# Kernel optimization log

Hardware: AMD Instinct MI355X
Metric: run time of the kernel (lower is better)

## Reference

```python
import jax, jax.numpy as jnp
import numpy as np
from jax import lax

SEQ_LEN, BATCH, POSE, H, PRED_LEN = 32, 32768, 34, 16, 15


def setup_inputs() -> dict:
    key = jax.random.key(0)
    ks = jax.random.split(key, 22)
    w = lambda k, s: (jax.random.normal(k, s, jnp.float32) * 0.1)
    return {
        "obs_s": jax.random.normal(ks[0], (SEQ_LEN, BATCH, POSE), jnp.float32),
        "enc_Wih": w(ks[1], (4 * H, POSE)), "enc_Whh": w(ks[2], (4 * H, H)),
        "enc_bih": w(ks[3], (4 * H,)), "enc_bhh": w(ks[4], (4 * H,)),
        "dec_Wih": w(ks[5], (4 * H, POSE)), "dec_Whh": w(ks[6], (4 * H, H)),
        "dec_bih": w(ks[7], (4 * H,)), "dec_bhh": w(ks[8], (4 * H,)),
        "cr_Wih": w(ks[9], (4 * H, POSE)), "cr_Whh": w(ks[10], (4 * H, H)),
        "cr_bih": w(ks[11], (4 * H,)), "cr_bhh": w(ks[12], (4 * H,)),
        "fc_W": w(ks[13], (POSE, H)), "fc_b": w(ks[14], (POSE,)),
        "fcc_W": w(ks[15], (2, H)), "fcc_b": w(ks[16], (2,)),
        "mlp_W": w(ks[17], (H, H)), "mlp_b": w(ks[18], (H,)),
        "emb_W": w(ks[19], (POSE, 2)), "emb_b": w(ks[20], (POSE,)),
        "pred_len": PRED_LEN,
    }


def _cell(x, h, c, Wih, Whh, bih, bhh):
    # torch LSTM gate order: i, f, g, o
    gates = x @ Wih.T + bih + h @ Whh.T + bhh  # [B, 4H]
    i, f, g, o = jnp.split(gates, 4, axis=-1)
    c = jax.nn.sigmoid(f) * c + jax.nn.sigmoid(i) * jnp.tanh(g)
    h = jax.nn.sigmoid(o) * jnp.tanh(c)
    return h, c


def reference(obs_s, enc_Wih, enc_Whh, enc_bih, enc_bhh,
              dec_Wih, dec_Whh, dec_bih, dec_bhh,
              cr_Wih, cr_Whh, cr_bih, cr_bhh,
              fc_W, fc_b, fcc_W, fcc_b, mlp_W, mlp_b, emb_W, emb_b,
              pred_len):
    batch = obs_s.shape[1]
    h0 = jnp.zeros((batch, H), obs_s.dtype)
    c0 = jnp.zeros((batch, H), obs_s.dtype)

    def enc_step(carry, x):
        h, c = _cell(x, *carry, enc_Wih, enc_Whh, enc_bih, enc_bhh)
        return (h, c), None

    (h, c), _ = lax.scan(enc_step, (h0, c0), obs_s)

    hc = h @ mlp_W.T + mlp_b           # crossing hidden init from encoder h
    cc = jnp.zeros_like(hc)
    last_s = obs_s[-1]                 # [B, POSE]
    last_cr = obs_s[-1]

    def dec_step(carry, _):
        h, c, hc, cc, last_s, last_cr = carry
        hc, cc = _cell(last_cr, hc, cc, cr_Wih, cr_Whh, cr_bih, cr_bhh)
        curr_cr = jax.nn.softmax(hc @ fcc_W.T + fcc_b, axis=-1)   # [B, 2]
        next_cr = curr_cr @ emb_W.T + emb_b                        # [B, POSE]
        h, c = _cell(last_s, h, c, dec_Wih, dec_Whh, dec_bih, dec_bhh)
        curr_s = h @ fc_W.T + fc_b                                 # [B, POSE]
        return (h, c, hc, cc, curr_s, next_cr), (curr_s, curr_cr)

    _, (pred_s, pred_crossing) = lax.scan(
        dec_step, (h, c, hc, cc, last_s, last_cr), None, length=pred_len)
    return pred_s, pred_crossing
```

## Files before the change

### kernel.cpp

```cpp
#include <hip/hip_runtime.h>
#include <cstddef>

#define SEQLEN 32
#define BATCH  32768
#define POSE   34
#define PREDL  15
#define LOG2E  1.4426950408889634f
#define K2E    2.8853901817779268f

typedef __attribute__((ext_vector_type(8))) short short8;
typedef __attribute__((ext_vector_type(4))) float f32x4;
typedef union { short8 s8; unsigned u[4]; } pk8;

#define MF(a,b,c) __builtin_amdgcn_mfma_f32_16x16x32_bf16(a,b,c,0,0,0)
#define EXP2(x)  __builtin_amdgcn_exp2f(x)
#define RCP(x)   __builtin_amdgcn_rcpf(x)

__device__ __forceinline__ unsigned short f2bf(float f){ __bf16 b=(__bf16)f; return __builtin_bit_cast(unsigned short,b); }
__device__ __forceinline__ unsigned f22bf(float lo,float hi){ return (unsigned)f2bf(lo) | ((unsigned)f2bf(hi)<<16); }
__device__ __forceinline__ short8 zero8(){ pk8 r; r.u[0]=0;r.u[1]=0;r.u[2]=0;r.u[3]=0; return r.s8; }
__device__ __forceinline__ float scGT(int gt){ return (gt==2)?K2E:LOG2E; }

__device__ __forceinline__ short8 g8s(const float* __restrict__ p, float s){
    pk8 r;
    r.u[0]=f22bf(p[0]*s,p[1]*s); r.u[1]=f22bf(p[2]*s,p[3]*s);
    r.u[2]=f22bf(p[4]*s,p[5]*s); r.u[3]=f22bf(p[6]*s,p[7]*s);
    return r.s8;
}

__device__ __forceinline__ void pw4v(const f32x4 (&ac)[4], f32x4 &cs,
                                     unsigned &hp0, unsigned &hp1){
    f32x4 A,C,B,O;
#pragma unroll
    for(int j=0;j<4;++j){
        A[j]=EXP2(-ac[0][j]); C[j]=EXP2(-ac[1][j]);
        B[j]=EXP2( ac[2][j]); O[j]=EXP2(-ac[3][j]);
    }
    const f32x4 one={1.f,1.f,1.f,1.f};
    f32x4 u=one+A, w=one+C, v=B+one, Bm=B-one;
    f32x4 t1=u*v;
    f32x4 num=cs*t1+Bm*w;
    f32x4 den=t1*w;
    f32x4 rd_,E,rh;
#pragma unroll
    for(int j=0;j<4;++j) rd_[j]=RCP(den[j]);
    f32x4 cn=num*rd_;
    cs=cn;
#pragma unroll
    for(int j=0;j<4;++j) E[j]=EXP2(K2E*cn[j]);
    f32x4 hd=(one+O)*(E+one);
#pragma unroll
    for(int j=0;j<4;++j) rh[j]=RCP(hd[j]);
    f32x4 hv=(E-one)*rh;
    hp0=f22bf(hv[0],hv[1]); hp1=f22bf(hv[2],hv[3]);
}

extern "C" __global__ void lstm_prep(
    const float* __restrict__ dWih, const float* __restrict__ dWhh,
    const float* __restrict__ dbih, const float* __restrict__ dbhh,
    const float* __restrict__ cWih, const float* __restrict__ cWhh,
    const float* __restrict__ cbih, const float* __restrict__ cbhh,
    const float* __restrict__ fcW,  const float* __restrict__ fcb,
    const float* __restrict__ embW, const float* __restrict__ embb,
    float* __restrict__ wsBD, float* __restrict__ wsBC,
    unsigned short* __restrict__ wsDh, unsigned short* __restrict__ wsCh,
    unsigned short* __restrict__ wsCp)
{
    int idx = blockIdx.x*256 + threadIdx.x;
    if(idx < 1024){
        int R=idx>>4, k=idx&15;
        float s=scGT(R>>4);
        float vD=dWhh[R*16+k];
        for(int p=0;p<34;++p) vD=fmaf(dWih[R*34+p],fcW[p*16+k],vD);
        wsDh[idx]=f2bf(vD*s);
        wsCh[idx]=f2bf(cWhh[R*16+k]*s);
    }
    if(idx < 128){
        int R=idx>>1, k=idx&1;
        float s=scGT(R>>4);
        float v=0.f;
        for(int p=0;p<34;++p) v=fmaf(cWih[R*34+p],embW[2*p+k],v);
        wsCp[idx]=f2bf(v*s);
    }
    if(idx < 64){
        int R=idx;
        float s=scGT(R>>4);
        float vD=dbih[R]+dbhh[R], vC=cbih[R]+cbhh[R];
        for(int p=0;p<34;++p){ vD=fmaf(dWih[R*34+p],fcb[p],vD); vC=fmaf(cWih[R*34+p],embb[p],vC); }
        wsBD[idx]=vD*s; wsBC[idx]=vC*s;
    }
}

extern "C" __global__ void __launch_bounds__(256,2) lstm_w7(
    const float* __restrict__ obs_s,
    const float* __restrict__ eWih, const float* __restrict__ eWhh,
    const float* __restrict__ ebih, const float* __restrict__ ebhh,
    const float* __restrict__ dWih, const float* __restrict__ dWhh,
    const float* __restrict__ dbih, const float* __restrict__ dbhh,
    const float* __restrict__ cWih, const float* __restrict__ cWhh,
    const float* __restrict__ cbih, const float* __restrict__ cbhh,
    const float* __restrict__ fcW,  const float* __restrict__ fcb,
    const float* __restrict__ fccW, const float* __restrict__ fccb,
    const float* __restrict__ mlpW, const float* __restrict__ mlpb,
    const float* __restrict__ wsBD, const float* __restrict__ wsBC,
    const unsigned short* __restrict__ wsDh, const unsigned short* __restrict__ wsCh,
    const unsigned short* __restrict__ wsCp,
    float* __restrict__ out_s, float* __restrict__ out_cr)
{
    __shared__ unsigned xt4[4][4][320];

    const int tid=threadIdx.x;
    const int l=tid&63;
    const int wv=tid>>6;
    const int lo=l&15, g=l>>4;
    const int pb=blockIdx.x*64 + wv*16;
    unsigned* XT=&xt4[wv][0][0];

    unsigned pofs[5]; int wofs[5];
#pragma unroll
    for(int it=0; it<5; ++it){
        int i2=l+64*it;
        int r=i2/17, w=i2-r*17;
        pofs[it]=(unsigned)((pb+r)*17+w);
        wofs[it]=r*20+w;
    }

    short8 wEx[4], wEhT[4]; f32x4 biasE[4];
#pragma unroll
    for(int gt=0;gt<4;++gt){
        float s=scGT(gt);
        int R=gt*16+lo;
        wEx[gt]=g8s(&eWih[R*34+8*g], s);
        pk8 r2;
        r2.u[0]=f22bf(eWhh[R*16+4*g]*s,   eWhh[R*16+4*g+1]*s);
        r2.u[1]=f22bf(eWhh[R*16+4*g+2]*s, eWhh[R*16+4*g+3]*s);
        r2.u[2]=(g==0)? f22bf(eWih[R*34+32]*s, eWih[R*34+33]*s) : 0u;
        r2.u[3]=0u;
        wEhT[gt]=r2.s8;
        float4 ba=*(const float4*)&ebih[gt*16+4*g];
        float4 bb=*(const float4*)&ebhh[gt*16+4*g];
        biasE[gt]=f32x4{(ba.x+bb.x)*s,(ba.y+bb.y)*s,(ba.z+bb.z)*s,(ba.w+bb.w)*s};
    }

    f32x4 cS={0.f,0.f,0.f,0.f};
    unsigned hp0=0u, hp1=0u;

    float2 RA[4][5];
    auto ldblk=[&](float2 (&R)[4][5], int t0){
#pragma unroll
        for(int s=0;s<4;++s){
            const float2* base=(const float2*)obs_s + (size_t)(t0+s)*(BATCH*17);
#pragma unroll
            for(int it=0;it<5;++it)
                if(it<4 || l<16) R[s][it]=base[pofs[it]];
        }
    };
    auto wrblk=[&](const float2 (&R)[4][5]){
#pragma unroll
        for(int s=0;s<4;++s)
#pragma unroll
            for(int it=0;it<5;++it)
                if(it<4 || l<16) XT[s*320+wofs[it]]=f22bf(R[s][it].x,R[s][it].y);
    };

    short8 fbQ=zero8(); unsigned ftQ=0u;
    ldblk(RA,0);
#pragma unroll 1
    for(int kb=0;kb<8;++kb){
        wrblk(RA);
        if(kb+1<8) ldblk(RA,4*(kb+1));
        short8 bx[4]; unsigned tw[4];
#pragma unroll
        for(int s=0;s<4;++s){
            bx[s]=*(const short8*)&XT[s*320+lo*20+4*g];
            tw[s]=XT[s*320+lo*20+16];
        }
        f32x4 cx[4][4];
#pragma unroll
        for(int s=0;s<4;++s)
#pragma unroll
            for(int gt=0;gt<4;++gt)
                cx[s][gt]=MF(wEx[gt],bx[s],biasE[gt]);
        fbQ=bx[3]; ftQ=tw[3];
#pragma unroll
        for(int s=0;s<4;++s){
            pk8 bh; bh.u[0]=hp0; bh.u[1]=hp1; bh.u[2]=(g==0)?tw[s]:0u; bh.u[3]=0u;
            f32x4 acc[4];
#pragma unroll
            for(int gt=0;gt<4;++gt) acc[gt]=MF(wEhT[gt],bh.s8,cx[s][gt]);
            pw4v(acc,cS,hp0,hp1);
        }
    }

    short8 wDh[4], wCA[4]; f32x4 biasD[4], biasC[4];
#pragma unroll
    for(int gt=0;gt<4;++gt){
        int R=gt*16+lo;
        uint2 qd=*(const uint2*)&wsDh[R*16+4*g];
        pk8 rd; rd.u[0]=qd.x; rd.u[1]=qd.y; rd.u[2]=0u; rd.u[3]=0u;
        wDh[gt]=rd.s8;
        uint2 qc=*(const uint2*)&wsCh[R*16+4*g];
        pk8 rc; rc.u[0]=qc.x; rc.u[1]=qc.y;
        rc.u[2]=(g==0)? *(const unsigned*)&wsCp[R*2] : 0u; rc.u[3]=0u;
        wCA[gt]=rc.s8;
        biasD[gt]=*(const f32x4*)&wsBD[gt*16+4*g];
        biasC[gt]=*(const f32x4*)&wsBC[gt*16+4*g];
    }
    short8 wF[3]; f32x4 fcbF[3];
#pragma unroll
    for(int nt=0;nt<3;++nt){
        int np=nt*16+lo;
        if(np<POSE){
            pk8 r;
            r.u[0]=f22bf(fcW[np*16+4*g],   fcW[np*16+4*g+1]);
            r.u[1]=f22bf(fcW[np*16+4*g+2], fcW[np*16+4*g+3]);
            r.u[2]=0u; r.u[3]=0u;
            wF[nt]=r.s8;
        } else wF[nt]=zero8();
#pragma unroll
        for(int j=0;j<4;++j){
            int row=nt*16+4*g+j;
            fcbF[nt][j]=(row<POSE)? fcb[row] : 0.f;
        }
    }
    short8 wFC, wM; f32x4 fccC, mlpbF;
    if(lo<2){
        pk8 r;
        r.u[0]=f22bf(fccW[lo*16+4*g],   fccW[lo*16+4*g+1]);
        r.u[1]=f22bf(fccW[lo*16+4*g+2], fccW[lo*16+4*g+3]);
        r.u[2]=0u; r.u[3]=0u; wFC=r.s8;
    } else wFC=zero8();
    fccC=(g==0)? f32x4{fccb[0],fccb[1],0.f,0.f} : f32x4{0.f,0.f,0.f,0.f};
    {
        pk8 r;
        r.u[0]=f22bf(mlpW[lo*16+4*g],   mlpW[lo*16+4*g+1]);
        r.u[1]=f22bf(mlpW[lo*16+4*g+2], mlpW[lo*16+4*g+3]);
        r.u[2]=0u; r.u[3]=0u; wM=r.s8;
        mlpbF=*(const f32x4*)&mlpb[4*g];
    }

    unsigned hcp0,hcp1;
    {
        pk8 bh; bh.u[0]=hp0; bh.u[1]=hp1; bh.u[2]=0u; bh.u[3]=0u;
        f32x4 o=MF(wM,bh.s8,mlpbF);
        hcp0=f22bf(o[0],o[1]); hcp1=f22bf(o[2],o[3]);
    }
    f32x4 cC={0.f,0.f,0.f,0.f};
    unsigned pp=0u;

    auto dec_tail=[&](int s, const f32x4 (&aC)[4], const f32x4 (&aD)[4]){
        pw4v(aD,cS,hp0,hp1);
        pw4v(aC,cC,hcp0,hcp1);
        pk8 bhc; bhc.u[0]=hcp0; bhc.u[1]=hcp1; bhc.u[2]=0u; bhc.u[3]=0u;
        f32x4 zz=MF(wFC,bhc.s8,fccC);
        float z0=zz[0], z1=zz[1];
        float mx=fmaxf(z0,z1);
        float e0=EXP2(LOG2E*(z0-mx)), e1=EXP2(LOG2E*(z1-mx));
        float rs=RCP(e0+e1);
        float p0=e0*rs, p1=e1*rs;
        unsigned ppn=f22bf(p0,p1);
        if(g==0)
            ((float2*)out_cr)[(size_t)s*BATCH+pb+lo]=make_float2(p0,p1);
        pp=(unsigned)__shfl((int)ppn, lo, 64);
        pk8 bh; bh.u[0]=hp0; bh.u[1]=hp1; bh.u[2]=0u; bh.u[3]=0u;
        float* po = out_s + ((size_t)s*BATCH + pb + lo)*POSE;
        f32x4 o0=MF(wF[0],bh.s8,fcbF[0]);
        f32x4 o1=MF(wF[1],bh.s8,fcbF[1]);
        *(float2*)(po+4*g)     =make_float2(o0[0],o0[1]);
        *(float2*)(po+4*g+2)   =make_float2(o0[2],o0[3]);
        *(float2*)(po+16+4*g)  =make_float2(o1[0],o1[1]);
        *(float2*)(po+16+4*g+2)=make_float2(o1[2],o1[3]);
        f32x4 o2=MF(wF[2],bh.s8,fcbF[2]);
        if(g==0) *(float2*)(po+32)=make_float2(o2[0],o2[1]);
    };

    {
        f32x4 aC[4], aD[4];
#pragma unroll
        for(int gt=0;gt<4;++gt){
            float s=scGT(gt);
            int R=gt*16+lo;
            short8 a1=g8s(&cWih[R*34+8*g], s);
            pk8 a2;
            a2.u[0]=f22bf(cWhh[R*16+4*g]*s,   cWhh[R*16+4*g+1]*s);
            a2.u[1]=f22bf(cWhh[R*16+4*g+2]*s, cWhh[R*16+4*g+3]*s);
            a2.u[2]=(g==0)? f22bf(cWih[R*34+32]*s, cWih[R*34+33]*s) : 0u;
            a2.u[3]=0u;
            float4 ba=*(const float4*)&cbih[gt*16+4*g];
            float4 bb=*(const float4*)&cbhh[gt*16+4*g];
            f32x4 bc0={(ba.x+bb.x)*s,(ba.y+bb.y)*s,(ba.z+bb.z)*s,(ba.w+bb.w)*s};
            pk8 bhc; bhc.u[0]=hcp0; bhc.u[1]=hcp1; bhc.u[2]=(g==0)?ftQ:0u; bhc.u[3]=0u;
            f32x4 cx=MF(a1,fbQ,bc0);
            aC[gt]=MF(a2.s8,bhc.s8,cx);
            short8 d1=g8s(&dWih[R*34+8*g], s);
            pk8 d2;
            d2.u[0]=f22bf(dWhh[R*16+4*g]*s,   dWhh[R*16+4*g+1]*s);
            d2.u[1]=f22bf(dWhh[R*16+4*g+2]*s, dWhh[R*16+4*g+3]*s);
            d2.u[2]=(g==0)? f22bf(dWih[R*34+32]*s, dWih[R*34+33]*s) : 0u;
            d2.u[3]=0u;
            float4 da=*(const float4*)&dbih[gt*16+4*g];
            float4 db=*(const float4*)&dbhh[gt*16+4*g];
            f32x4 bd0={(da.x+db.x)*s,(da.y+db.y)*s,(da.z+db.z)*s,(da.w+db.w)*s};
            pk8 bhd; bhd.u[0]=hp0; bhd.u[1]=hp1; bhd.u[2]=(g==0)?ftQ:0u; bhd.u[3]=0u;
            f32x4 dx=MF(d1,fbQ,bd0);
            aD[gt]=MF(d2.s8,bhd.s8,dx);
        }
        dec_tail(0,aC,aD);
    }
#pragma unroll 1
    for(int s=1;s<PREDL;++s){
        pk8 bd; bd.u[0]=hp0; bd.u[1]=hp1; bd.u[2]=0u; bd.u[3]=0u;
        pk8 bc; bc.u[0]=hcp0; bc.u[1]=hcp1; bc.u[2]=(g==0)?pp:0u; bc.u[3]=0u;
        f32x4 aC[4], aD[4];
#pragma unroll
        for(int gt=0;gt<4;++gt) aD[gt]=MF(wDh[gt],bd.s8,biasD[gt]);
#pragma unroll
        for(int gt=0;gt<4;++gt) aC[gt]=MF(wCA[gt],bc.s8,biasC[gt]);
        dec_tail(s,aC,aD);
    }
}

extern "C" void kernel_launch(void* const* d_in, const int* in_sizes, int n_in,
                              void* d_out, int out_size, void* d_ws, size_t ws_size,
                              hipStream_t stream)
{
    const float* obs  = (const float*)d_in[0];
    const float* eWih = (const float*)d_in[1];
    const float* eWhh = (const float*)d_in[2];
    const float* ebih = (const float*)d_in[3];
    const float* ebhh = (const float*)d_in[4];
    const float* dWih = (const float*)d_in[5];
    const float* dWhh = (const float*)d_in[6];
    const float* dbih = (const float*)d_in[7];
    const float* dbhh = (const float*)d_in[8];
    const float* cWih = (const float*)d_in[9];
    const float* cWhh = (const float*)d_in[10];
    const float* cbih = (const float*)d_in[11];
    const float* cbhh = (const float*)d_in[12];
    const float* fcW  = (const float*)d_in[13];
    const float* fcb  = (const float*)d_in[14];
    const float* fccW = (const float*)d_in[15];
    const float* fccb = (const float*)d_in[16];
    const float* mlpW = (const float*)d_in[17];
    const float* mlpb = (const float*)d_in[18];
    const float* embW = (const float*)d_in[19];
    const float* embb = (const float*)d_in[20];

    float* out_s  = (float*)d_out;
    float* out_cr = out_s + (size_t)PREDL*BATCH*POSE;

    float* wsBD = (float*)d_ws;
    float* wsBC = wsBD + 64;
    unsigned short* wsDh = (unsigned short*)(wsBC+64);
    unsigned short* wsCh = wsDh + 1024;
    unsigned short* wsCp = wsCh + 1024;

    hipLaunchKernelGGL(lstm_prep, dim3(4), dim3(256), 0, stream,
                       dWih, dWhh, dbih, dbhh, cWih, cWhh, cbih, cbhh,
                       fcW, fcb, embW, embb, wsBD, wsBC, wsDh, wsCh, wsCp);
    hipLaunchKernelGGL(lstm_w7, dim3(BATCH/64), dim3(256), 0, stream,
                       obs, eWih, eWhh, ebih, ebhh, dWih, dWhh, dbih, dbhh,
                       cWih, cWhh, cbih, cbhh, fcW, fcb, fccW, fccb,
                       mlpW, mlpb, wsBD, wsBC, wsDh, wsCh, wsCp,
                       out_s, out_cr);
}
```

Baseline: 66.67 us.

## Process two independent 16-row batch chunks per wave to interleave LSTM recurrences

Each wave now handles two 16-sample chunks instead of one, so the grid shrinks to half the blocks and the recurrent MFMA and pointwise gate chains of the two chunks are interleaved. This is meant to hide the serial latency of the per-step MFMA to exp/rcp to MFMA dependency chain through instruction-level parallelism within a wave. The cost is more registers (launch bounds drop to one block per SIMD pair), fewer resident waves, and a different observation load and LDS staging layout (two timesteps per block instead of four).

```diff
diff --git a/kernel.cpp b/kernel.cpp
--- a/kernel.cpp
+++ b/kernel.cpp
@@ -28,31 +28,36 @@
     return r.s8;
 }
 
-__device__ __forceinline__ void pw4v(const f32x4 (&ac)[4], f32x4 &cs,
-                                     unsigned &hp0, unsigned &hp1){
-    f32x4 A,C,B,O;
+__device__ __forceinline__ void pw4v2(const f32x4 (&ac)[2][4], f32x4 (&cs)[2],
+                                      unsigned (&hp0)[2], unsigned (&hp1)[2]){
+    f32x4 A[2],C[2],B[2],O[2];
+#pragma unroll
+    for(int ch=0;ch<2;++ch)
 #pragma unroll
     for(int j=0;j<4;++j){
-        A[j]=EXP2(-ac[0][j]); C[j]=EXP2(-ac[1][j]);
-        B[j]=EXP2( ac[2][j]); O[j]=EXP2(-ac[3][j]);
+        A[ch][j]=EXP2(-ac[ch][0][j]); C[ch][j]=EXP2(-ac[ch][1][j]);
+        B[ch][j]=EXP2( ac[ch][2][j]); O[ch][j]=EXP2(-ac[ch][3][j]);
     }
     const f32x4 one={1.f,1.f,1.f,1.f};
-    f32x4 u=one+A, w=one+C, v=B+one, Bm=B-one;
-    f32x4 t1=u*v;
-    f32x4 num=cs*t1+Bm*w;
-    f32x4 den=t1*w;
-    f32x4 rd_,E,rh;
-#pragma unroll
-    for(int j=0;j<4;++j) rd_[j]=RCP(den[j]);
-    f32x4 cn=num*rd_;
-    cs=cn;
-#pragma unroll
-    for(int j=0;j<4;++j) E[j]=EXP2(K2E*cn[j]);
-    f32x4 hd=(one+O)*(E+one);
-#pragma unroll
-    for(int j=0;j<4;++j) rh[j]=RCP(hd[j]);
-    f32x4 hv=(E-one)*rh;
-    hp0=f22bf(hv[0],hv[1]); hp1=f22bf(hv[2],hv[3]);
+#pragma unroll
+    for(int ch=0;ch<2;++ch){
+        f32x4 u=one+A[ch], w=one+C[ch], v=B[ch]+one, Bm=B[ch]-one;
+        f32x4 t1=u*v;
+        f32x4 num=cs[ch]*t1+Bm*w;
+        f32x4 den=t1*w;
+        f32x4 rd_,E,rh;
+#pragma unroll
+        for(int j=0;j<4;++j) rd_[j]=RCP(den[j]);
+        f32x4 cn=num*rd_;
+        cs[ch]=cn;
+#pragma unroll
+        for(int j=0;j<4;++j) E[j]=EXP2(K2E*cn[j]);
+        f32x4 hd=(one+O[ch])*(E+one);
+#pragma unroll
+        for(int j=0;j<4;++j) rh[j]=RCP(hd[j]);
+        f32x4 hv=(E-one)*rh;
+        hp0[ch]=f22bf(hv[0],hv[1]); hp1[ch]=f22bf(hv[2],hv[3]);
+    }
 }
 
 extern "C" __global__ void lstm_prep(
@@ -91,7 +96,7 @@
     }
 }
 
-extern "C" __global__ void __launch_bounds__(256,2) lstm_w7(
+extern "C" __global__ void __launch_bounds__(256,1) lstm_w8(
     const float* __restrict__ obs_s,
     const float* __restrict__ eWih, const float* __restrict__ eWhh,
     const float* __restrict__ ebih, const float* __restrict__ ebhh,
@@ -107,14 +112,14 @@
     const unsigned short* __restrict__ wsCp,
     float* __restrict__ out_s, float* __restrict__ out_cr)
 {
-    __shared__ unsigned xt4[4][4][320];
+    __shared__ unsigned xt4[4][2][2][320];
 
     const int tid=threadIdx.x;
     const int l=tid&63;
     const int wv=tid>>6;
     const int lo=l&15, g=l>>4;
-    const int pb=blockIdx.x*64 + wv*16;
-    unsigned* XT=&xt4[wv][0][0];
+    const int pb=blockIdx.x*128 + wv*32;
+    unsigned (*XT)[2][320]=xt4[wv];
 
     unsigned pofs[5]; int wofs[5];
 #pragma unroll
@@ -142,53 +147,67 @@
         biasE[gt]=f32x4{(ba.x+bb.x)*s,(ba.y+bb.y)*s,(ba.z+bb.z)*s,(ba.w+bb.w)*s};
     }
 
-    f32x4 cS={0.f,0.f,0.f,0.f};
-    unsigned hp0=0u, hp1=0u;
-
-    float2 RA[4][5];
-    auto ldblk=[&](float2 (&R)[4][5], int t0){
-#pragma unroll
-        for(int s=0;s<4;++s){
-            const float2* base=(const float2*)obs_s + (size_t)(t0+s)*(BATCH*17);
+    f32x4 cS[2]={{0.f,0.f,0.f,0.f},{0.f,0.f,0.f,0.f}};
+    unsigned hp0[2]={0u,0u}, hp1[2]={0u,0u};
+
+    float2 RA[2][2][5];
+    auto ldblk=[&](int t0){
+#pragma unroll
+        for(int s2=0;s2<2;++s2){
+            const float2* base=(const float2*)obs_s + (size_t)(t0+s2)*(BATCH*17);
+#pragma unroll
+            for(int ch=0;ch<2;++ch)
 #pragma unroll
             for(int it=0;it<5;++it)
-                if(it<4 || l<16) R[s][it]=base[pofs[it]];
+                if(it<4 || l<16) RA[ch][s2][it]=base[pofs[it]+ch*272u];
         }
     };
-    auto wrblk=[&](const float2 (&R)[4][5]){
-#pragma unroll
-        for(int s=0;s<4;++s)
-#pragma unroll
-            for(int it=0;it<5;++it)
-                if(it<4 || l<16) XT[s*320+wofs[it]]=f22bf(R[s][it].x,R[s][it].y);
+    auto wrblk=[&](){
+#pragma unroll
+        for(int ch=0;ch<2;++ch)
+#pragma unroll
+        for(int s2=0;s2<2;++s2)
+#pragma unroll
+        for(int it=0;it<5;++it)
+            if(it<4 || l<16) XT[ch][s2][wofs[it]]=f22bf(RA[ch][s2][it].x,RA[ch][s2][it].y);
     };
 
-    short8 fbQ=zero8(); unsigned ftQ=0u;
-    ldblk(RA,0);
+    short8 fbQ[2]; unsigned ftQ[2];
+    fbQ[0]=zero8(); fbQ[1]=zero8(); ftQ[0]=0u; ftQ[1]=0u;
+    ldblk(0);
 #pragma unroll 1
-    for(int kb=0;kb<8;++kb){
-        wrblk(RA);
-        if(kb+1<8) ldblk(RA,4*(kb+1));
-        short8 bx[4]; unsigned tw[4];
-#pragma unroll
-        for(int s=0;s<4;++s){
-            bx[s]=*(const short8*)&XT[s*320+lo*20+4*g];
-            tw[s]=XT[s*320+lo*20+16];
-        }
-        f32x4 cx[4][4];
-#pragma unroll
-        for(int s=0;s<4;++s)
-#pragma unroll
-            for(int gt=0;gt<4;++gt)
-                cx[s][gt]=MF(wEx[gt],bx[s],biasE[gt]);
-        fbQ=bx[3]; ftQ=tw[3];
-#pragma unroll
-        for(int s=0;s<4;++s){
-            pk8 bh; bh.u[0]=hp0; bh.u[1]=hp1; bh.u[2]=(g==0)?tw[s]:0u; bh.u[3]=0u;
-            f32x4 acc[4];
-#pragma unroll
-            for(int gt=0;gt<4;++gt) acc[gt]=MF(wEhT[gt],bh.s8,cx[s][gt]);
-            pw4v(acc,cS,hp0,hp1);
+    for(int kb=0;kb<16;++kb){
+        wrblk();
+        if(kb+1<16) ldblk(2*(kb+1));
+        short8 bx[2][2]; unsigned tw[2][2];
+#pragma unroll
+        for(int ch=0;ch<2;++ch)
+#pragma unroll
+        for(int s2=0;s2<2;++s2){
+            bx[ch][s2]=*(const short8*)&XT[ch][s2][lo*20+4*g];
+            tw[ch][s2]=XT[ch][s2][lo*20+16];
+        }
+        f32x4 cx[2][2][4];
+#pragma unroll
+        for(int ch=0;ch<2;++ch)
+#pragma unroll
+        for(int s2=0;s2<2;++s2)
+#pragma unroll
+        for(int gt=0;gt<4;++gt)
+            cx[ch][s2][gt]=MF(wEx[gt],bx[ch][s2],biasE[gt]);
+        fbQ[0]=bx[0][1]; ftQ[0]=tw[0][1];
+        fbQ[1]=bx[1][1]; ftQ[1]=tw[1][1];
+#pragma unroll
+        for(int s2=0;s2<2;++s2){
+            f32x4 acc[2][4];
+#pragma unroll
+            for(int ch=0;ch<2;++ch){
+                pk8 bh; bh.u[0]=hp0[ch]; bh.u[1]=hp1[ch];
+                bh.u[2]=(g==0)?tw[ch][s2]:0u; bh.u[3]=0u;
+#pragma unroll
+                for(int gt=0;gt<4;++gt) acc[ch][gt]=MF(wEhT[gt],bh.s8,cx[ch][s2][gt]);
+            }
+            pw4v2(acc,cS,hp0,hp1);
         }
     }
 
@@ -239,83 +258,104 @@
         mlpbF=*(const f32x4*)&mlpb[4*g];
     }
 
-    unsigned hcp0,hcp1;
+    unsigned hcp0[2],hcp1[2];
+#pragma unroll
+    for(int ch=0;ch<2;++ch){
+        pk8 bh; bh.u[0]=hp0[ch]; bh.u[1]=hp1[ch]; bh.u[2]=0u; bh.u[3]=0u;
+        f32x4 o=MF(wM,bh.s8,mlpbF);
+        hcp0[ch]=f22bf(o[0],o[1]); hcp1[ch]=f22bf(o[2],o[3]);
+    }
+    f32x4 cC[2]={{0.f,0.f,0.f,0.f},{0.f,0.f,0.f,0.f}};
+    unsigned pp[2]={0u,0u};
+
+    auto dec_tail=[&](int s, const f32x4 (&aC)[2][4], const f32x4 (&aD)[2][4]){
+        pw4v2(aD,cS,hp0,hp1);
+        pw4v2(aC,cC,hcp0,hcp1);
+#pragma unroll
+        for(int ch=0;ch<2;++ch){
+            const int pbc=pb+16*ch;
+            pk8 bhc; bhc.u[0]=hcp0[ch]; bhc.u[1]=hcp1[ch]; bhc.u[2]=0u; bhc.u[3]=0u;
+            f32x4 zz=MF(wFC,bhc.s8,fccC);
+            float z0=zz[0], z1=zz[1];
+            float mx=fmaxf(z0,z1);
+            float e0=EXP2(LOG2E*(z0-mx)), e1=EXP2(LOG2E*(z1-mx));
+            float rs=RCP(e0+e1);
+            float p0=e0*rs, p1=e1*rs;
+            unsigned ppn=f22bf(p0,p1);
+            if(g==0)
+                ((float2*)out_cr)[(size_t)s*BATCH+pbc+lo]=make_float2(p0,p1);
+            pp[ch]=(unsigned)__shfl((int)ppn, lo, 64);
+            pk8 bh; bh.u[0]=hp0[ch]; bh.u[1]=hp1[ch]; bh.u[2]=0u; bh.u[3]=0u;
+            float* po = out_s + ((size_t)s*BATCH + pbc + lo)*POSE;
+            f32x4 o0=MF(wF[0],bh.s8,fcbF[0]);
+            f32x4 o1=MF(wF[1],bh.s8,fcbF[1]);
+            *(float2*)(po+4*g)     =make_float2(o0[0],o0[1]);
+            *(float2*)(po+4*g+2)   =make_float2(o0[2],o0[3]);
+            *(float2*)(po+16+4*g)  =make_float2(o1[0],o1[1]);
+            *(float2*)(po+16+4*g+2)=make_float2(o1[2],o1[3]);
+            f32x4 o2=MF(wF[2],bh.s8,fcbF[2]);
+            if(g==0) *(float2*)(po+32)=make_float2(o2[0],o2[1]);
+        }
+    };
+
     {
-        pk8 bh; bh.u[0]=hp0; bh.u[1]=hp1; bh.u[2]=0u; bh.u[3]=0u;
-        f32x4 o=MF(wM,bh.s8,mlpbF);
-        hcp0=f22bf(o[0],o[1]); hcp1=f22bf(o[2],o[3]);
-    }
-    f32x4 cC={0.f,0.f,0.f,0.f};
-    unsigned pp=0u;
-
-    auto dec_tail=[&](int s, const f32x4 (&aC)[4], const f32x4 (&aD)[4]){
-        pw4v(aD,cS,hp0,hp1);
-        pw4v(aC,cC,hcp0,hcp1);
-        pk8 bhc; bhc.u[0]=hcp0; bhc.u[1]=hcp1; bhc.u[2]=0u; bhc.u[3]=0u;
-        f32x4 zz=MF(wFC,bhc.s8,fccC);
-        float z0=zz[0], z1=zz[1];
-        float mx=fmaxf(z0,z1);
-        float e0=EXP2(LOG2E*(z0-mx)), e1=EXP2(LOG2E*(z1-mx));
-        float rs=RCP(e0+e1);
-        float p0=e0*rs, p1=e1*rs;
-        unsigned ppn=f22bf(p0,p1);
-        if(g==0)
-            ((float2*)out_cr)[(size_t)s*BATCH+pb+lo]=make_float2(p0,p1);
-        pp=(unsigned)__shfl((int)ppn, lo, 64);
-        pk8 bh; bh.u[0]=hp0; bh.u[1]=hp1; bh.u[2]=0u; bh.u[3]=0u;
-        float* po = out_s + ((size_t)s*BATCH + pb + lo)*POSE;
-        f32x4 o0=MF(wF[0],bh.s8,fcbF[0]);
-        f32x4 o1=MF(wF[1],bh.s8,fcbF[1]);
-        *(float2*)(po+4*g)     =make_float2(o0[0],o0[1]);
-        *(float2*)(po+4*g+2)   =make_float2(o0[2],o0[3]);
-        *(float2*)(po+16+4*g)  =make_float2(o1[0],o1[1]);
-        *(float2*)(po+16+4*g+2)=make_float2(o1[2],o1[3]);
-        f32x4 o2=MF(wF[2],bh.s8,fcbF[2]);
-        if(g==0) *(float2*)(po+32)=make_float2(o2[0],o2[1]);
-    };
-
-    {
-        f32x4 aC[4], aD[4];
+        short8 a1c[4],a2c[4],a1d[4],a2d[4]; f32x4 bc0[4],bd0[4];
 #pragma unroll
         for(int gt=0;gt<4;++gt){
-            float s=scGT(gt);
+            float sgt=scGT(gt);
             int R=gt*16+lo;
-            short8 a1=g8s(&cWih[R*34+8*g], s);
+            a1c[gt]=g8s(&cWih[R*34+8*g], sgt);
             pk8 a2;
-            a2.u[0]=f22bf(cWhh[R*16+4*g]*s,   cWhh[R*16+4*g+1]*s);
-            a2.u[1]=f22bf(cWhh[R*16+4*g+2]*s, cWhh[R*16+4*g+3]*s);
-            a2.u[2]=(g==0)? f22bf(cWih[R*34+32]*s, cWih[R*34+33]*s) : 0u;
+            a2.u[0]=f22bf(cWhh[R*16+4*g]*sgt,   cWhh[R*16+4*g+1]*sgt);
+            a2.u[1]=f22bf(cWhh[R*16+4*g+2]*sgt, cWhh[R*16+4*g+3]*sgt);
+            a2.u[2]=(g==0)? f22bf(cWih[R*34+32]*sgt, cWih[R*34+33]*sgt) : 0u;
             a2.u[3]=0u;
+            a2c[gt]=a2.s8;
             float4 ba=*(const float4*)&cbih[gt*16+4*g];
             float4 bb=*(const float4*)&cbhh[gt*16+4*g];
-            f32x4 bc0={(ba.x+bb.x)*s,(ba.y+bb.y)*s,(ba.z+bb.z)*s,(ba.w+bb.w)*s};
-            pk8 bhc; bhc.u[0]=hcp0; bhc.u[1]=hcp1; bhc.u[2]=(g==0)?ftQ:0u; bhc.u[3]=0u;
-            f32x4 cx=MF(a1,fbQ,bc0);
-            aC[gt]=MF(a2.s8,bhc.s8,cx);
-            short8 d1=g8s(&dWih[R*34+8*g], s);
+            bc0[gt]=f32x4{(ba.x+bb.x)*sgt,(ba.y+bb.y)*sgt,(ba.z+bb.z)*sgt,(ba.w+bb.w)*sgt};
+            a1d[gt]=g8s(&dWih[R*34+8*g], sgt);
             pk8 d2;
-            d2.u[0]=f22bf(dWhh[R*16+4*g]*s,   dWhh[R*16+4*g+1]*s);
-            d2.u[1]=f22bf(dWhh[R*16+4*g+2]*s, dWhh[R*16+4*g+3]*s);
-            d2.u[2]=(g==0)? f22bf(dWih[R*34+32]*s, dWih[R*34+33]*s) : 0u;
+            d2.u[0]=f22bf(dWhh[R*16+4*g]*sgt,   dWhh[R*16+4*g+1]*sgt);
+            d2.u[1]=f22bf(dWhh[R*16+4*g+2]*sgt, dWhh[R*16+4*g+3]*sgt);
+            d2.u[2]=(g==0)? f22bf(dWih[R*34+32]*sgt, dWih[R*34+33]*sgt) : 0u;
             d2.u[3]=0u;
+            a2d[gt]=d2.s8;
             float4 da=*(const float4*)&dbih[gt*16+4*g];
             float4 db=*(const float4*)&dbhh[gt*16+4*g];
-            f32x4 bd0={(da.x+db.x)*s,(da.y+db.y)*s,(da.z+db.z)*s,(da.w+db.w)*s};
-            pk8 bhd; bhd.u[0]=hp0; bhd.u[1]=hp1; bhd.u[2]=(g==0)?ftQ:0u; bhd.u[3]=0u;
-            f32x4 dx=MF(d1,fbQ,bd0);
-            aD[gt]=MF(d2.s8,bhd.s8,dx);
+            bd0[gt]=f32x4{(da.x+db.x)*sgt,(da.y+db.y)*sgt,(da.z+db.z)*sgt,(da.w+db.w)*sgt};
+        }
+        f32x4 aC[2][4], aD[2][4];
+#pragma unroll
+        for(int ch=0;ch<2;++ch){
+            pk8 bhc; bhc.u[0]=hcp0[ch]; bhc.u[1]=hcp1[ch];
+            bhc.u[2]=(g==0)?ftQ[ch]:0u; bhc.u[3]=0u;
+            pk8 bhd; bhd.u[0]=hp0[ch]; bhd.u[1]=hp1[ch];
+            bhd.u[2]=(g==0)?ftQ[ch]:0u; bhd.u[3]=0u;
+#pragma unroll
+            for(int gt=0;gt<4;++gt){
+                f32x4 cxx=MF(a1c[gt],fbQ[ch],bc0[gt]);
+                aC[ch][gt]=MF(a2c[gt],bhc.s8,cxx);
+                f32x4 dxx=MF(a1d[gt],fbQ[ch],bd0[gt]);
+                aD[ch][gt]=MF(a2d[gt],bhd.s8,dxx);
+            }
         }
         dec_tail(0,aC,aD);
     }
 #pragma unroll 1
     for(int s=1;s<PREDL;++s){
-        pk8 bd; bd.u[0]=hp0; bd.u[1]=hp1; bd.u[2]=0u; bd.u[3]=0u;
-        pk8 bc; bc.u[0]=hcp0; bc.u[1]=hcp1; bc.u[2]=(g==0)?pp:0u; bc.u[3]=0u;
-        f32x4 aC[4], aD[4];
-#pragma unroll
-        for(int gt=0;gt<4;++gt) aD[gt]=MF(wDh[gt],bd.s8,biasD[gt]);
-#pragma unroll
-        for(int gt=0;gt<4;++gt) aC[gt]=MF(wCA[gt],bc.s8,biasC[gt]);
+        f32x4 aC[2][4], aD[2][4];
+#pragma unroll
+        for(int ch=0;ch<2;++ch){
+            pk8 bd; bd.u[0]=hp0[ch]; bd.u[1]=hp1[ch]; bd.u[2]=0u; bd.u[3]=0u;
+            pk8 bc; bc.u[0]=hcp0[ch]; bc.u[1]=hcp1[ch];
+            bc.u[2]=(g==0)?pp[ch]:0u; bc.u[3]=0u;
+#pragma unroll
+            for(int gt=0;gt<4;++gt){
+                aD[ch][gt]=MF(wDh[gt],bd.s8,biasD[gt]);
+                aC[ch][gt]=MF(wCA[gt],bc.s8,biasC[gt]);
+            }
+        }
         dec_tail(s,aC,aD);
     }
 }
@@ -358,7 +398,7 @@
     hipLaunchKernelGGL(lstm_prep, dim3(4), dim3(256), 0, stream,
                        dWih, dWhh, dbih, dbhh, cWih, cWhh, cbih, cbhh,
                        fcW, fcb, embW, embb, wsBD, wsBC, wsDh, wsCh, wsCp);
-    hipLaunchKernelGGL(lstm_w7, dim3(BATCH/64), dim3(256), 0, stream,
+    hipLaunchKernelGGL(lstm_w8, dim3(BATCH/128), dim3(256), 0, stream,
                        obs, eWih, eWhh, ebih, ebhh, dWih, dWhh, dbih, dbhh,
                        cWih, cWhh, cbih, cbhh, fcW, fcb, fccW, fccb,
                        mlpW, mlpb, wsBD, wsBC, wsDh, wsCh, wsCp,
```

Result: slower. 74.79 us (+12.2%).

## Split encoder and decoder kernels; run decoder and crossing LSTMs on separate waves

Applied to the files above, without the earlier changes.

The fused kernel is split in two. An encoder kernel also runs the weight-prep work in one extra block and writes each lane's h, hc and c state to workspace. A decoder kernel then gives the decoder LSTM and the crossing LSTM to different wavefronts, so their two independent recurrences run in parallel across twice as many waves. This doubles the decoder grid and shortens the serial chain per wave. The cost is a global round-trip for the state, an extra launch boundary, and a re-read of the last observation frame.

```diff
diff --git a/kernel.cpp b/kernel.cpp
--- a/kernel.cpp
+++ b/kernel.cpp
@@ -55,7 +55,11 @@
     hp0=f22bf(hv[0],hv[1]); hp1=f22bf(hv[2],hv[3]);
 }
 
-extern "C" __global__ void lstm_prep(
+extern "C" __global__ void __launch_bounds__(256,2) lstm_enc(
+    const float* __restrict__ obs_s,
+    const float* __restrict__ eWih, const float* __restrict__ eWhh,
+    const float* __restrict__ ebih, const float* __restrict__ ebhh,
+    const float* __restrict__ mlpW, const float* __restrict__ mlpb,
     const float* __restrict__ dWih, const float* __restrict__ dWhh,
     const float* __restrict__ dbih, const float* __restrict__ dbhh,
     const float* __restrict__ cWih, const float* __restrict__ cWhh,
@@ -64,50 +68,35 @@
     const float* __restrict__ embW, const float* __restrict__ embb,
     float* __restrict__ wsBD, float* __restrict__ wsBC,
     unsigned short* __restrict__ wsDh, unsigned short* __restrict__ wsCh,
-    unsigned short* __restrict__ wsCp)
-{
-    int idx = blockIdx.x*256 + threadIdx.x;
-    if(idx < 1024){
-        int R=idx>>4, k=idx&15;
-        float s=scGT(R>>4);
-        float vD=dWhh[R*16+k];
-        for(int p=0;p<34;++p) vD=fmaf(dWih[R*34+p],fcW[p*16+k],vD);
-        wsDh[idx]=f2bf(vD*s);
-        wsCh[idx]=f2bf(cWhh[R*16+k]*s);
-    }
-    if(idx < 128){
-        int R=idx>>1, k=idx&1;
-        float s=scGT(R>>4);
-        float v=0.f;
-        for(int p=0;p<34;++p) v=fmaf(cWih[R*34+p],embW[2*p+k],v);
-        wsCp[idx]=f2bf(v*s);
-    }
-    if(idx < 64){
-        int R=idx;
-        float s=scGT(R>>4);
-        float vD=dbih[R]+dbhh[R], vC=cbih[R]+cbhh[R];
-        for(int p=0;p<34;++p){ vD=fmaf(dWih[R*34+p],fcb[p],vD); vC=fmaf(cWih[R*34+p],embb[p],vC); }
-        wsBD[idx]=vD*s; wsBC[idx]=vC*s;
-    }
-}
-
-extern "C" __global__ void __launch_bounds__(256,2) lstm_w7(
-    const float* __restrict__ obs_s,
-    const float* __restrict__ eWih, const float* __restrict__ eWhh,
-    const float* __restrict__ ebih, const float* __restrict__ ebhh,
-    const float* __restrict__ dWih, const float* __restrict__ dWhh,
-    const float* __restrict__ dbih, const float* __restrict__ dbhh,
-    const float* __restrict__ cWih, const float* __restrict__ cWhh,
-    const float* __restrict__ cbih, const float* __restrict__ cbhh,
-    const float* __restrict__ fcW,  const float* __restrict__ fcb,
-    const float* __restrict__ fccW, const float* __restrict__ fccb,
-    const float* __restrict__ mlpW, const float* __restrict__ mlpb,
-    const float* __restrict__ wsBD, const float* __restrict__ wsBC,
-    const unsigned short* __restrict__ wsDh, const unsigned short* __restrict__ wsCh,
-    const unsigned short* __restrict__ wsCp,
-    float* __restrict__ out_s, float* __restrict__ out_cr)
+    unsigned short* __restrict__ wsCp, unsigned* __restrict__ hand)
 {
     __shared__ unsigned xt4[4][4][320];
+
+    if(blockIdx.x>=512){
+        for(int idx=threadIdx.x; idx<1024; idx+=256){
+            int R=idx>>4, k=idx&15;
+            float s=scGT(R>>4);
+            float vD=dWhh[R*16+k];
+            for(int p=0;p<34;++p) vD=fmaf(dWih[R*34+p],fcW[p*16+k],vD);
+            wsDh[idx]=f2bf(vD*s);
+            wsCh[idx]=f2bf(cWhh[R*16+k]*s);
+        }
+        for(int idx=threadIdx.x; idx<128; idx+=256){
+            int R=idx>>1, k=idx&1;
+            float s=scGT(R>>4);
+            float v=0.f;
+            for(int p=0;p<34;++p) v=fmaf(cWih[R*34+p],embW[2*p+k],v);
+            wsCp[idx]=f2bf(v*s);
+        }
+        for(int idx=threadIdx.x; idx<64; idx+=256){
+            int R=idx;
+            float s=scGT(R>>4);
+            float vD=dbih[R]+dbhh[R], vC=cbih[R]+cbhh[R];
+            for(int p=0;p<34;++p){ vD=fmaf(dWih[R*34+p],fcb[p],vD); vC=fmaf(cWih[R*34+p],embb[p],vC); }
+            wsBD[idx]=vD*s; wsBC[idx]=vC*s;
+        }
+        return;
+    }
 
     const int tid=threadIdx.x;
     const int l=tid&63;
@@ -146,29 +135,28 @@
     unsigned hp0=0u, hp1=0u;
 
     float2 RA[4][5];
-    auto ldblk=[&](float2 (&R)[4][5], int t0){
+    auto ldblk=[&](int t0){
 #pragma unroll
         for(int s=0;s<4;++s){
             const float2* base=(const float2*)obs_s + (size_t)(t0+s)*(BATCH*17);
 #pragma unroll
             for(int it=0;it<5;++it)
-                if(it<4 || l<16) R[s][it]=base[pofs[it]];
+                if(it<4 || l<16) RA[s][it]=base[pofs[it]];
         }
     };
-    auto wrblk=[&](const float2 (&R)[4][5]){
+    auto wrblk=[&](){
 #pragma unroll
         for(int s=0;s<4;++s)
 #pragma unroll
             for(int it=0;it<5;++it)
-                if(it<4 || l<16) XT[s*320+wofs[it]]=f22bf(R[s][it].x,R[s][it].y);
+                if(it<4 || l<16) XT[s*320+wofs[it]]=f22bf(RA[s][it].x,RA[s][it].y);
     };
 
-    short8 fbQ=zero8(); unsigned ftQ=0u;
-    ldblk(RA,0);
+    ldblk(0);
 #pragma unroll 1
     for(int kb=0;kb<8;++kb){
-        wrblk(RA);
-        if(kb+1<8) ldblk(RA,4*(kb+1));
+        wrblk();
+        if(kb+1<8) ldblk(4*(kb+1));
         short8 bx[4]; unsigned tw[4];
 #pragma unroll
         for(int s=0;s<4;++s){
@@ -181,7 +169,6 @@
 #pragma unroll
             for(int gt=0;gt<4;++gt)
                 cx[s][gt]=MF(wEx[gt],bx[s],biasE[gt]);
-        fbQ=bx[3]; ftQ=tw[3];
 #pragma unroll
         for(int s=0;s<4;++s){
             pk8 bh; bh.u[0]=hp0; bh.u[1]=hp1; bh.u[2]=(g==0)?tw[s]:0u; bh.u[3]=0u;
@@ -192,131 +179,188 @@
         }
     }
 
-    short8 wDh[4], wCA[4]; f32x4 biasD[4], biasC[4];
-#pragma unroll
-    for(int gt=0;gt<4;++gt){
-        int R=gt*16+lo;
-        uint2 qd=*(const uint2*)&wsDh[R*16+4*g];
-        pk8 rd; rd.u[0]=qd.x; rd.u[1]=qd.y; rd.u[2]=0u; rd.u[3]=0u;
-        wDh[gt]=rd.s8;
-        uint2 qc=*(const uint2*)&wsCh[R*16+4*g];
-        pk8 rc; rc.u[0]=qc.x; rc.u[1]=qc.y;
-        rc.u[2]=(g==0)? *(const unsigned*)&wsCp[R*2] : 0u; rc.u[3]=0u;
-        wCA[gt]=rc.s8;
-        biasD[gt]=*(const f32x4*)&wsBD[gt*16+4*g];
-        biasC[gt]=*(const f32x4*)&wsBC[gt*16+4*g];
-    }
-    short8 wF[3]; f32x4 fcbF[3];
-#pragma unroll
-    for(int nt=0;nt<3;++nt){
-        int np=nt*16+lo;
-        if(np<POSE){
-            pk8 r;
-            r.u[0]=f22bf(fcW[np*16+4*g],   fcW[np*16+4*g+1]);
-            r.u[1]=f22bf(fcW[np*16+4*g+2], fcW[np*16+4*g+3]);
-            r.u[2]=0u; r.u[3]=0u;
-            wF[nt]=r.s8;
-        } else wF[nt]=zero8();
-#pragma unroll
-        for(int j=0;j<4;++j){
-            int row=nt*16+4*g+j;
-            fcbF[nt][j]=(row<POSE)? fcb[row] : 0.f;
-        }
-    }
-    short8 wFC, wM; f32x4 fccC, mlpbF;
-    if(lo<2){
-        pk8 r;
-        r.u[0]=f22bf(fccW[lo*16+4*g],   fccW[lo*16+4*g+1]);
-        r.u[1]=f22bf(fccW[lo*16+4*g+2], fccW[lo*16+4*g+3]);
-        r.u[2]=0u; r.u[3]=0u; wFC=r.s8;
-    } else wFC=zero8();
-    fccC=(g==0)? f32x4{fccb[0],fccb[1],0.f,0.f} : f32x4{0.f,0.f,0.f,0.f};
+    unsigned hcp0,hcp1;
     {
         pk8 r;
         r.u[0]=f22bf(mlpW[lo*16+4*g],   mlpW[lo*16+4*g+1]);
         r.u[1]=f22bf(mlpW[lo*16+4*g+2], mlpW[lo*16+4*g+3]);
-        r.u[2]=0u; r.u[3]=0u; wM=r.s8;
-        mlpbF=*(const f32x4*)&mlpb[4*g];
-    }
-
-    unsigned hcp0,hcp1;
+        r.u[2]=0u; r.u[3]=0u;
+        f32x4 mb=*(const f32x4*)&mlpb[4*g];
+        pk8 bh; bh.u[0]=hp0; bh.u[1]=hp1; bh.u[2]=0u; bh.u[3]=0u;
+        f32x4 o=MF(r.s8,bh.s8,mb);
+        hcp0=f22bf(o[0],o[1]); hcp1=f22bf(o[2],o[3]);
+    }
+
+    unsigned* Hw = hand + ((size_t)(blockIdx.x*4+wv)*64 + l)*8;
+    Hw[0]=hp0; Hw[1]=hp1; Hw[2]=hcp0; Hw[3]=hcp1;
+    *(f32x4*)(Hw+4)=cS;
+}
+
+extern "C" __global__ void __launch_bounds__(256,2) lstm_dec(
+    const float* __restrict__ obs_s,
+    const float* __restrict__ dWih, const float* __restrict__ dWhh,
+    const float* __restrict__ dbih, const float* __restrict__ dbhh,
+    const float* __restrict__ cWih, const float* __restrict__ cWhh,
+    const float* __restrict__ cbih, const float* __restrict__ cbhh,
+    const float* __restrict__ fcW,  const float* __restrict__ fcb,
+    const float* __restrict__ fccW, const float* __restrict__ fccb,
+    const float* __restrict__ wsBD, const float* __restrict__ wsBC,
+    const unsigned short* __restrict__ wsDh, const unsigned short* __restrict__ wsCh,
+    const unsigned short* __restrict__ wsCp, const unsigned* __restrict__ hand,
+    float* __restrict__ out_s, float* __restrict__ out_cr)
+{
+    const int tid=threadIdx.x;
+    const int l=tid&63;
+    const int wv=tid>>6;
+    const int lo=l&15, g=l>>4;
+    const int grp=blockIdx.x*2+(wv>>1);
+    const int role=__builtin_amdgcn_readfirstlane(wv&1);
+    const int pb=grp*16;
+
+    const unsigned* H = hand + ((size_t)grp*64 + l)*8;
+    unsigned h0w=H[0], h1w=H[1], hc0w=H[2], hc1w=H[3];
+    f32x4 csIn=*(const f32x4*)(H+4);
+
+    const float* px=obs_s+((size_t)(SEQLEN-1)*BATCH+pb+lo)*POSE;
+    short8 fbQ;
     {
-        pk8 bh; bh.u[0]=hp0; bh.u[1]=hp1; bh.u[2]=0u; bh.u[3]=0u;
-        f32x4 o=MF(wM,bh.s8,mlpbF);
-        hcp0=f22bf(o[0],o[1]); hcp1=f22bf(o[2],o[3]);
-    }
-    f32x4 cC={0.f,0.f,0.f,0.f};
-    unsigned pp=0u;
-
-    auto dec_tail=[&](int s, const f32x4 (&aC)[4], const f32x4 (&aD)[4]){
-        pw4v(aD,cS,hp0,hp1);
-        pw4v(aC,cC,hcp0,hcp1);
-        pk8 bhc; bhc.u[0]=hcp0; bhc.u[1]=hcp1; bhc.u[2]=0u; bhc.u[3]=0u;
-        f32x4 zz=MF(wFC,bhc.s8,fccC);
-        float z0=zz[0], z1=zz[1];
-        float mx=fmaxf(z0,z1);
-        float e0=EXP2(LOG2E*(z0-mx)), e1=EXP2(LOG2E*(z1-mx));
-        float rs=RCP(e0+e1);
-        float p0=e0*rs, p1=e1*rs;
-        unsigned ppn=f22bf(p0,p1);
-        if(g==0)
-            ((float2*)out_cr)[(size_t)s*BATCH+pb+lo]=make_float2(p0,p1);
-        pp=(unsigned)__shfl((int)ppn, lo, 64);
-        pk8 bh; bh.u[0]=hp0; bh.u[1]=hp1; bh.u[2]=0u; bh.u[3]=0u;
-        float* po = out_s + ((size_t)s*BATCH + pb + lo)*POSE;
-        f32x4 o0=MF(wF[0],bh.s8,fcbF[0]);
-        f32x4 o1=MF(wF[1],bh.s8,fcbF[1]);
-        *(float2*)(po+4*g)     =make_float2(o0[0],o0[1]);
-        *(float2*)(po+4*g+2)   =make_float2(o0[2],o0[3]);
-        *(float2*)(po+16+4*g)  =make_float2(o1[0],o1[1]);
-        *(float2*)(po+16+4*g+2)=make_float2(o1[2],o1[3]);
-        f32x4 o2=MF(wF[2],bh.s8,fcbF[2]);
-        if(g==0) *(float2*)(po+32)=make_float2(o2[0],o2[1]);
-    };
-
-    {
-        f32x4 aC[4], aD[4];
+        const float2* p2=(const float2*)(px+8*g);
+        float2 q0=p2[0],q1=p2[1],q2=p2[2],q3=p2[3];
+        pk8 r;
+        r.u[0]=f22bf(q0.x,q0.y); r.u[1]=f22bf(q1.x,q1.y);
+        r.u[2]=f22bf(q2.x,q2.y); r.u[3]=f22bf(q3.x,q3.y);
+        fbQ=r.s8;
+    }
+    unsigned ftQ=f22bf(px[32],px[33]);
+
+    if(role==0){
+        f32x4 cS=csIn;
+        unsigned hp0=h0w, hp1=h1w;
+        f32x4 aD[4];
+        {
+#pragma unroll
+            for(int gt=0;gt<4;++gt){
+                float s=scGT(gt);
+                int R=gt*16+lo;
+                short8 d1=g8s(&dWih[R*34+8*g], s);
+                pk8 d2;
+                d2.u[0]=f22bf(dWhh[R*16+4*g]*s,   dWhh[R*16+4*g+1]*s);
+                d2.u[1]=f22bf(dWhh[R*16+4*g+2]*s, dWhh[R*16+4*g+3]*s);
+                d2.u[2]=(g==0)? f22bf(dWih[R*34+32]*s, dWih[R*34+33]*s) : 0u;
+                d2.u[3]=0u;
+                float4 da=*(const float4*)&dbih[gt*16+4*g];
+                float4 db=*(const float4*)&dbhh[gt*16+4*g];
+                f32x4 bd0={(da.x+db.x)*s,(da.y+db.y)*s,(da.z+db.z)*s,(da.w+db.w)*s};
+                pk8 bhd; bhd.u[0]=hp0; bhd.u[1]=hp1; bhd.u[2]=(g==0)?ftQ:0u; bhd.u[3]=0u;
+                f32x4 dx=MF(d1,fbQ,bd0);
+                aD[gt]=MF(d2.s8,bhd.s8,dx);
+            }
+        }
+        short8 wF[3]; f32x4 fcbF[3];
+#pragma unroll
+        for(int nt=0;nt<3;++nt){
+            int np=nt*16+lo;
+            if(np<POSE){
+                pk8 r;
+                r.u[0]=f22bf(fcW[np*16+4*g],   fcW[np*16+4*g+1]);
+                r.u[1]=f22bf(fcW[np*16+4*g+2], fcW[np*16+4*g+3]);
+                r.u[2]=0u; r.u[3]=0u;
+                wF[nt]=r.s8;
+            } else wF[nt]=zero8();
+#pragma unroll
+            for(int j=0;j<4;++j){
+                int row=nt*16+4*g+j;
+                fcbF[nt][j]=(row<POSE)? fcb[row] : 0.f;
+            }
+        }
+        short8 wDh[4]; f32x4 biasD[4];
 #pragma unroll
         for(int gt=0;gt<4;++gt){
-            float s=scGT(gt);
             int R=gt*16+lo;
-            short8 a1=g8s(&cWih[R*34+8*g], s);
-            pk8 a2;
-            a2.u[0]=f22bf(cWhh[R*16+4*g]*s,   cWhh[R*16+4*g+1]*s);
-            a2.u[1]=f22bf(cWhh[R*16+4*g+2]*s, cWhh[R*16+4*g+3]*s);
-            a2.u[2]=(g==0)? f22bf(cWih[R*34+32]*s, cWih[R*34+33]*s) : 0u;
-            a2.u[3]=0u;
-            float4 ba=*(const float4*)&cbih[gt*16+4*g];
-            float4 bb=*(const float4*)&cbhh[gt*16+4*g];
-            f32x4 bc0={(ba.x+bb.x)*s,(ba.y+bb.y)*s,(ba.z+bb.z)*s,(ba.w+bb.w)*s};
-            pk8 bhc; bhc.u[0]=hcp0; bhc.u[1]=hcp1; bhc.u[2]=(g==0)?ftQ:0u; bhc.u[3]=0u;
-            f32x4 cx=MF(a1,fbQ,bc0);
-            aC[gt]=MF(a2.s8,bhc.s8,cx);
-            short8 d1=g8s(&dWih[R*34+8*g], s);
-            pk8 d2;
-            d2.u[0]=f22bf(dWhh[R*16+4*g]*s,   dWhh[R*16+4*g+1]*s);
-            d2.u[1]=f22bf(dWhh[R*16+4*g+2]*s, dWhh[R*16+4*g+3]*s);
-            d2.u[2]=(g==0)? f22bf(dWih[R*34+32]*s, dWih[R*34+33]*s) : 0u;
-            d2.u[3]=0u;
-            float4 da=*(const float4*)&dbih[gt*16+4*g];
-            float4 db=*(const float4*)&dbhh[gt*16+4*g];
-            f32x4 bd0={(da.x+db.x)*s,(da.y+db.y)*s,(da.z+db.z)*s,(da.w+db.w)*s};
-            pk8 bhd; bhd.u[0]=hp0; bhd.u[1]=hp1; bhd.u[2]=(g==0)?ftQ:0u; bhd.u[3]=0u;
-            f32x4 dx=MF(d1,fbQ,bd0);
-            aD[gt]=MF(d2.s8,bhd.s8,dx);
-        }
-        dec_tail(0,aC,aD);
-    }
+            uint2 qd=*(const uint2*)&wsDh[R*16+4*g];
+            pk8 rd; rd.u[0]=qd.x; rd.u[1]=qd.y; rd.u[2]=0u; rd.u[3]=0u;
+            wDh[gt]=rd.s8;
+            biasD[gt]=*(const f32x4*)&wsBD[gt*16+4*g];
+        }
 #pragma unroll 1
-    for(int s=1;s<PREDL;++s){
-        pk8 bd; bd.u[0]=hp0; bd.u[1]=hp1; bd.u[2]=0u; bd.u[3]=0u;
-        pk8 bc; bc.u[0]=hcp0; bc.u[1]=hcp1; bc.u[2]=(g==0)?pp:0u; bc.u[3]=0u;
-        f32x4 aC[4], aD[4];
-#pragma unroll
-        for(int gt=0;gt<4;++gt) aD[gt]=MF(wDh[gt],bd.s8,biasD[gt]);
-#pragma unroll
-        for(int gt=0;gt<4;++gt) aC[gt]=MF(wCA[gt],bc.s8,biasC[gt]);
-        dec_tail(s,aC,aD);
+        for(int s=0;s<PREDL;++s){
+            pw4v(aD,cS,hp0,hp1);
+            pk8 bh; bh.u[0]=hp0; bh.u[1]=hp1; bh.u[2]=0u; bh.u[3]=0u;
+            f32x4 o0=MF(wF[0],bh.s8,fcbF[0]);
+            f32x4 o1=MF(wF[1],bh.s8,fcbF[1]);
+            f32x4 o2=MF(wF[2],bh.s8,fcbF[2]);
+            float* po = out_s + ((size_t)s*BATCH + pb + lo)*POSE;
+            *(float2*)(po+4*g)     =make_float2(o0[0],o0[1]);
+            *(float2*)(po+4*g+2)   =make_float2(o0[2],o0[3]);
+            *(float2*)(po+16+4*g)  =make_float2(o1[0],o1[1]);
+            *(float2*)(po+16+4*g+2)=make_float2(o1[2],o1[3]);
+            if(g==0) *(float2*)(po+32)=make_float2(o2[0],o2[1]);
+            if(s+1<PREDL){
+#pragma unroll
+                for(int gt=0;gt<4;++gt) aD[gt]=MF(wDh[gt],bh.s8,biasD[gt]);
+            }
+        }
+    } else {
+        f32x4 cC={0.f,0.f,0.f,0.f};
+        unsigned hcp0=hc0w, hcp1=hc1w, pp=0u;
+        f32x4 aC[4];
+        {
+#pragma unroll
+            for(int gt=0;gt<4;++gt){
+                float s=scGT(gt);
+                int R=gt*16+lo;
+                short8 a1=g8s(&cWih[R*34+8*g], s);
+                pk8 a2;
+                a2.u[0]=f22bf(cWhh[R*16+4*g]*s,   cWhh[R*16+4*g+1]*s);
+                a2.u[1]=f22bf(cWhh[R*16+4*g+2]*s, cWhh[R*16+4*g+3]*s);
+                a2.u[2]=(g==0)? f22bf(cWih[R*34+32]*s, cWih[R*34+33]*s) : 0u;
+                a2.u[3]=0u;
+                float4 ba=*(const float4*)&cbih[gt*16+4*g];
+                float4 bb=*(const float4*)&cbhh[gt*16+4*g];
+                f32x4 bc0={(ba.x+bb.x)*s,(ba.y+bb.y)*s,(ba.z+bb.z)*s,(ba.w+bb.w)*s};
+                pk8 bhc; bhc.u[0]=hcp0; bhc.u[1]=hcp1; bhc.u[2]=(g==0)?ftQ:0u; bhc.u[3]=0u;
+                f32x4 cx=MF(a1,fbQ,bc0);
+                aC[gt]=MF(a2.s8,bhc.s8,cx);
+            }
+        }
+        short8 wFC; f32x4 fccC;
+        if(lo<2){
+            pk8 r;
+            r.u[0]=f22bf(fccW[lo*16+4*g],   fccW[lo*16+4*g+1]);
+            r.u[1]=f22bf(fccW[lo*16+4*g+2], fccW[lo*16+4*g+3]);
+            r.u[2]=0u; r.u[3]=0u; wFC=r.s8;
+        } else wFC=zero8();
+        fccC=(g==0)? f32x4{fccb[0],fccb[1],0.f,0.f} : f32x4{0.f,0.f,0.f,0.f};
+        short8 wCA[4]; f32x4 biasC[4];
+#pragma unroll
+        for(int gt=0;gt<4;++gt){
+            int R=gt*16+lo;
+            uint2 qc=*(const uint2*)&wsCh[R*16+4*g];
+            pk8 rc; rc.u[0]=qc.x; rc.u[1]=qc.y;
+            rc.u[2]=(g==0)? *(const unsigned*)&wsCp[R*2] : 0u; rc.u[3]=0u;
+            wCA[gt]=rc.s8;
+            biasC[gt]=*(const f32x4*)&wsBC[gt*16+4*g];
+        }
+#pragma unroll 1
+        for(int s=0;s<PREDL;++s){
+            pw4v(aC,cC,hcp0,hcp1);
+            pk8 bhc2; bhc2.u[0]=hcp0; bhc2.u[1]=hcp1; bhc2.u[2]=0u; bhc2.u[3]=0u;
+            f32x4 zz=MF(wFC,bhc2.s8,fccC);
+            float z0=zz[0], z1=zz[1];
+            float mx=fmaxf(z0,z1);
+            float e0=EXP2(LOG2E*(z0-mx)), e1=EXP2(LOG2E*(z1-mx));
+            float rs=RCP(e0+e1);
+            float p0=e0*rs, p1=e1*rs;
+            unsigned ppn=f22bf(p0,p1);
+            if(g==0)
+                ((float2*)out_cr)[(size_t)s*BATCH+pb+lo]=make_float2(p0,p1);
+            pp=(unsigned)__shfl((int)ppn, lo, 64);
+            if(s+1<PREDL){
+                pk8 bc; bc.u[0]=hcp0; bc.u[1]=hcp1; bc.u[2]=(g==0)?pp:0u; bc.u[3]=0u;
+#pragma unroll
+                for(int gt=0;gt<4;++gt) aC[gt]=MF(wCA[gt],bc.s8,biasC[gt]);
+            }
+        }
     }
 }
 
@@ -354,13 +398,16 @@
     unsigned short* wsDh = (unsigned short*)(wsBC+64);
     unsigned short* wsCh = wsDh + 1024;
     unsigned short* wsCp = wsCh + 1024;
-
-    hipLaunchKernelGGL(lstm_prep, dim3(4), dim3(256), 0, stream,
+    unsigned* hand = (unsigned*)((char*)d_ws + 8192);
+
+    hipLaunchKernelGGL(lstm_enc, dim3(513), dim3(256), 0, stream,
+                       obs, eWih, eWhh, ebih, ebhh, mlpW, mlpb,
                        dWih, dWhh, dbih, dbhh, cWih, cWhh, cbih, cbhh,
-                       fcW, fcb, embW, embb, wsBD, wsBC, wsDh, wsCh, wsCp);
-    hipLaunchKernelGGL(lstm_w7, dim3(BATCH/64), dim3(256), 0, stream,
-                       obs, eWih, eWhh, ebih, ebhh, dWih, dWhh, dbih, dbhh,
-                       cWih, cWhh, cbih, cbhh, fcW, fcb, fccW, fccb,
-                       mlpW, mlpb, wsBD, wsBC, wsDh, wsCh, wsCp,
+                       fcW, fcb, embW, embb,
+                       wsBD, wsBC, wsDh, wsCh, wsCp, hand);
+    hipLaunchKernelGGL(lstm_dec, dim3(BATCH/32), dim3(256), 0, stream,
+                       obs, dWih, dWhh, dbih, dbhh, cWih, cWhh, cbih, cbhh,
+                       fcW, fcb, fccW, fccb,
+                       wsBD, wsBC, wsDh, wsCh, wsCp, hand,
                        out_s, out_cr);
 }
```

Result: no change. 65.45 us (-1.8%).
